# Optimization experiments

Hardware: AMD Instinct MI355X
Metric: run time of the kernel (lower is better)

The kernel has to match this reference:

```python
import jax, jax.numpy as jnp
import numpy as np

B, S, MM_DIM = 64, 512, 1024
HID, T, NL, NHEAD = 512, 4, 4, 8
DH = HID // NHEAD
RQ_L, CB = 3, 256
EPS = 1e-5


def setup_inputs() -> dict:
    key = jax.random.key(0)
    ks = jax.random.split(key, 24)
    n = jax.random.normal
    d = dict(
        multimodal_features=n(ks[0], (B, S, MM_DIM), jnp.float32),
        proj_W=n(ks[1], (MM_DIM, HID), jnp.float32) * 0.02,
        proj_b=jnp.zeros((HID,), jnp.float32),
        query_tokens=n(ks[2], (T, HID), jnp.float32),
        Wq=n(ks[3], (NL, HID, HID), jnp.float32) * 0.02,
        bq=jnp.zeros((NL, HID), jnp.float32),
        Wk=n(ks[4], (NL, HID, HID), jnp.float32) * 0.02,
        bk=jnp.zeros((NL, HID), jnp.float32),
        Wv=n(ks[5], (NL, HID, HID), jnp.float32) * 0.02,
        bv=jnp.zeros((NL, HID), jnp.float32),
        Wo=n(ks[6], (NL, HID, HID), jnp.float32) * 0.02,
        bo=jnp.zeros((NL, HID), jnp.float32),
        W1=n(ks[7], (NL, HID, 4 * HID), jnp.float32) * 0.02,
        b1=jnp.zeros((NL, 4 * HID), jnp.float32),
        W2=n(ks[8], (NL, 4 * HID, HID), jnp.float32) * 0.02,
        b2=jnp.zeros((NL, HID), jnp.float32),
        ln_g=jnp.ones((NL, HID), jnp.float32),
        ln_b=jnp.zeros((NL, HID), jnp.float32),
        codebooks=n(ks[9], (RQ_L, CB, HID), jnp.float32),
    )
    return d


def _layernorm(x, g, b):
    mu = jnp.mean(x, axis=-1, keepdims=True)
    var = jnp.mean(jnp.square(x - mu), axis=-1, keepdims=True)
    return (x - mu) * jax.lax.rsqrt(var + EPS) * g + b


def _cross_attn(q, kv, Wq, bq, Wk, bk, Wv, bv, Wo, bo):
    Bq, Tq, _ = q.shape
    Sk = kv.shape[1]
    qh = (q @ Wq + bq).reshape(Bq, Tq, NHEAD, DH)
    kh = (kv @ Wk + bk).reshape(Bq, Sk, NHEAD, DH)
    vh = (kv @ Wv + bv).reshape(Bq, Sk, NHEAD, DH)
    scores = jnp.einsum('bthd,bshd->bhts', qh, kh) / np.sqrt(DH).astype(np.float32)
    attn = jax.nn.softmax(scores, axis=-1)
    out = jnp.einsum('bhts,bshd->bthd', attn, vh).reshape(Bq, Tq, NHEAD * DH)
    return out @ Wo + bo


def reference(multimodal_features, proj_W, proj_b, query_tokens,
              Wq, bq, Wk, bk, Wv, bv, Wo, bo, W1, b1, W2, b2,
              ln_g, ln_b, codebooks):
    x = multimodal_features @ proj_W + proj_b            # [B,S,HID]
    q = jnp.broadcast_to(query_tokens[None], (x.shape[0], T, HID))
    for i in range(NL):
        attn = _cross_attn(q, x, Wq[i], bq[i], Wk[i], bk[i], Wv[i], bv[i], Wo[i], bo[i])
        q = _layernorm(q + attn, ln_g[i], ln_b[i])
        ffn = jax.nn.gelu(q @ W1[i] + b1[i], approximate=False) @ W2[i] + b2[i]
        q = _layernorm(q + ffn, ln_g[i], ln_b[i])
    # residual quantization
    residual = q
    reconstructed = jnp.zeros_like(q)
    ids = []
    for l in range(RQ_L):
        cb = codebooks[l]                                # [CB,HID]
        d2 = (jnp.sum(residual * residual, axis=-1, keepdims=True)
              - 2.0 * (residual @ cb.T)
              + jnp.sum(cb * cb, axis=-1))               # [B,T,CB]
        idx = jnp.argmin(d2, axis=-1)                    # [B,T]
        ids.append(idx)
        cent = cb[idx]                                   # gather [B,T,HID]
        reconstructed = reconstructed + cent
        residual = residual - cent
    semantic_ids = jnp.stack(ids, axis=-1)               # [B,T,RQ_L]
    return semantic_ids, reconstructed
```

## Files before the change

kernel.cpp:

```cpp
#include <hip/hip_runtime.h>
#include <math.h>


typedef __attribute__((ext_vector_type(8))) short   s16x8;
typedef __attribute__((ext_vector_type(8))) __bf16  bf16x8;
typedef __attribute__((ext_vector_type(4))) float   f32x4;

__device__ __forceinline__ void split2(float v, unsigned short& hi, unsigned short& lo) {
    unsigned u = __builtin_bit_cast(unsigned, v);
    hi = (unsigned short)(u >> 16);
    float hf = __builtin_bit_cast(float, u & 0xffff0000u);
    float l = v - hf;
    unsigned ul = __builtin_bit_cast(unsigned, l);
    lo = (unsigned short)((ul + 0x7fffu + ((ul >> 16) & 1u)) >> 16);
}

__device__ __forceinline__ f32x4 mfma16(bf16x8 a, bf16x8 b, f32x4 c) {
    return __builtin_amdgcn_mfma_f32_16x16x32_bf16(a, b, c, 0, 0, 0);
}

__device__ __forceinline__ void gload16(const void* g, void* l) {
    __builtin_amdgcn_global_load_lds(
        (const __attribute__((address_space(1))) unsigned*)g,
        (__attribute__((address_space(3))) unsigned*)l, 16, 0, 0);
}

__device__ __forceinline__ bf16x8 bc16(const unsigned short* p) {
    return __builtin_bit_cast(bf16x8, *(const s16x8*)p);
}

template<int BM, int FM, int FN, int WR, int WC, int AMODE, int OMODE,
         int IDX, bool GELU, bool SWZ>
__global__ __launch_bounds__(256)
void mfma_gemm(const void* __restrict__ Ah_, const void* __restrict__ Al_,
               const unsigned short* __restrict__ Bh_, const unsigned short* __restrict__ Bl_,
               const float* __restrict__ bias,
               void* __restrict__ Ch_, void* __restrict__ Cl_,
               int K, int lda, int ldb, int ldc,
               long strA, long strB, long strC)
{
    constexpr int BHALF = 8192;
    constexpr int AHALF = 2 * BM * 32;
    __shared__ __align__(16) unsigned short sA[2 * AHALF];
    __shared__ __align__(16) unsigned short sB[2 * BHALF];

    int bx = blockIdx.x, by = blockIdx.y;
    if constexpr (SWZ) {
        int nb = gridDim.x * gridDim.y;
        int h  = bx + gridDim.x * by;
        int orig = (h & 7) * (nb >> 3) + (h >> 3);
        bx = orig % gridDim.x; by = orig / gridDim.x;
    }
    const int tid = threadIdx.x, z = blockIdx.z;
    const int m0 = by * BM, n0 = bx * 128;
    const int lane = tid & 63, w = tid >> 6;
    const int wr = w / WC, wc = w % WC;

    const float* Af = nullptr;
    const unsigned short *Ah = nullptr, *Al = nullptr;
    if constexpr (AMODE == 1) {
        Af = (const float*)Ah_;
    } else {
        Ah = (const unsigned short*)Ah_ + (long)z * strA;
        Al = (const unsigned short*)Al_ + (long)z * strA;
    }
    const unsigned short* Bh = Bh_ + (long)z * strB;
    const unsigned short* Bl = Bl_ + (long)z * strB;

    auto stageB = [&](int buf, int k0) {
#pragma unroll
        for (int i = 0; i < 4; i++) {
            const int c = tid + 256 * i;
            const int p = c >> 9, cc = c & 511, r = cc >> 2, sl = cc & 3;
            const int fs = (r + (r >> 2)) & 3;
            const unsigned short* g = (p ? Bl : Bh) + (long)(n0 + r) * ldb + k0 + ((sl ^ fs)) * 8;
            gload16(g, sB + buf * BHALF + p * 4096 + r * 32 + sl * 8);
        }
    };
    auto stageA = [&](int buf, int k0) {
        if constexpr (AMODE == 0 && BM == 32) {
            const int p = tid >> 7, c = tid & 127, r = c >> 2, sl = c & 3;
            const int fs = (r + (r >> 2)) & 3;
            const unsigned short* g = (p ? Al : Ah) + (long)(m0 + r) * lda + k0 + ((sl ^ fs)) * 8;
            gload16(g, sA + buf * AHALF + p * (BM * 32) + r * 32 + sl * 8);
        } else if constexpr (AMODE == 0 && BM == 16) {
            if (tid < 128) {
                const int p = tid >> 6, c = tid & 63, r = c >> 2, sl = c & 3;
                const int fs = (r + (r >> 2)) & 3;
                const unsigned short* g = (p ? Al : Ah) + (long)(m0 + r) * lda + k0 + ((sl ^ fs)) * 8;
                gload16(g, sA + buf * AHALF + p * (BM * 32) + r * 32 + sl * 8);
            }
        } else {
            const int r = tid >> 1, hh2 = tid & 1;
            const int fs = (r + (r >> 2)) & 3;
            const float* src = Af + (long)(m0 + r) * lda + k0 + hh2 * 16;
#pragma unroll
            for (int s2 = 0; s2 < 2; s2++) {
                const int s = 2 * hh2 + s2;
                float4 v0 = *(const float4*)(src + s2 * 8);
                float4 v1 = *(const float4*)(src + s2 * 8 + 4);
                float vv[8] = {v0.x, v0.y, v0.z, v0.w, v1.x, v1.y, v1.z, v1.w};
                union { s16x8 v; unsigned short u[8]; } hu, lu;
#pragma unroll
                for (int j = 0; j < 8; j++) split2(vv[j], hu.u[j], lu.u[j]);
                *(s16x8*)&sA[buf * AHALF + r * 32 + ((s ^ fs)) * 8] = hu.v;
                *(s16x8*)&sA[buf * AHALF + BM * 32 + r * 32 + ((s ^ fs)) * 8] = lu.v;
            }
        }
    };

    f32x4 acc[FM][FN];
#pragma unroll
    for (int i = 0; i < FM; i++)
#pragma unroll
        for (int j = 0; j < FN; j++) acc[i][j] = f32x4{0.f, 0.f, 0.f, 0.f};

    const int NT = K / 32;
    int buf = 0;
    stageB(0, 0);
    stageA(0, 0);
    __syncthreads();

    const int li = lane & 15, ks = lane >> 4;

    for (int kt = 0; kt < NT; kt++) {
        if (kt + 1 < NT) { stageB(buf ^ 1, (kt + 1) * 32); stageA(buf ^ 1, (kt + 1) * 32); }
        bf16x8 ah[FM], al[FM], bh[FN], bl[FN];
#pragma unroll
        for (int mi = 0; mi < FM; mi++) {
            const int r = wr * (FM * 16) + mi * 16 + li;
            const int fs = (r + (r >> 2)) & 3;
            ah[mi] = bc16(&sA[buf * AHALF + r * 32 + ((ks ^ fs)) * 8]);
            al[mi] = bc16(&sA[buf * AHALF + BM * 32 + r * 32 + ((ks ^ fs)) * 8]);
        }
#pragma unroll
        for (int ni = 0; ni < FN; ni++) {
            const int r = wc * (FN * 16) + ni * 16 + li;
            const int fs = (r + (r >> 2)) & 3;
            bh[ni] = bc16(&sB[buf * BHALF + r * 32 + ((ks ^ fs)) * 8]);
            bl[ni] = bc16(&sB[buf * BHALF + 4096 + r * 32 + ((ks ^ fs)) * 8]);
        }
#pragma unroll
        for (int mi = 0; mi < FM; mi++)
#pragma unroll
            for (int ni = 0; ni < FN; ni++) acc[mi][ni] = mfma16(ah[mi], bh[ni], acc[mi][ni]);
#pragma unroll
        for (int mi = 0; mi < FM; mi++)
#pragma unroll
            for (int ni = 0; ni < FN; ni++) acc[mi][ni] = mfma16(ah[mi], bl[ni], acc[mi][ni]);
#pragma unroll
        for (int mi = 0; mi < FM; mi++)
#pragma unroll
            for (int ni = 0; ni < FN; ni++) acc[mi][ni] = mfma16(al[mi], bh[ni], acc[mi][ni]);
        __syncthreads();
        buf ^= 1;
    }

#pragma unroll
    for (int mi = 0; mi < FM; mi++)
#pragma unroll
        for (int r4 = 0; r4 < 4; r4++) {
            const int m = m0 + wr * (FM * 16) + mi * 16 + (lane >> 4) * 4 + r4;
#pragma unroll
            for (int ni = 0; ni < FN; ni++) {
                const int n = n0 + wc * (FN * 16) + ni * 16 + (lane & 15);
                float v = acc[mi][ni][r4];
                if (bias) v += bias[n];
                if constexpr (GELU) v = 0.5f * v * (1.f + erff(v * 0.70710678118654752f));
                long id;
                if constexpr (IDX == 0)      id = (long)z * strC + (long)m * ldc + n;
                else                         id = ((long)(m >> 2)) * 16384
                                                + (long)((n >> 9) * 4 + (m & 3)) * 512 + (n & 511);
                if constexpr (OMODE == 1) {
                    unsigned short h, l; split2(v, h, l);
                    ((unsigned short*)Ch_)[id] = h;
                    ((unsigned short*)Cl_)[id] = l;
                } else {
                    ((float*)Ch_)[id] = v;
                }
            }
        }
}

__global__ __launch_bounds__(512)
void fused_attn(const unsigned short* __restrict__ A_h, const unsigned short* __restrict__ A_l,
                const unsigned short* __restrict__ x_h, const unsigned short* __restrict__ x_l,
                const unsigned short* __restrict__ xT_h, const unsigned short* __restrict__ xT_l,
                unsigned short* __restrict__ U_h, unsigned short* __restrict__ U_l)
{
    __shared__ __align__(16) unsigned short sB[2][2][8192];
    __shared__ __align__(16) unsigned short sA[2][2][512];
    __shared__ __align__(16) unsigned short sP[2][16][16][32];
    __shared__ float redm[8][16], reds[8][16];

    const int tid = threadIdx.x;
    const int lin  = blockIdx.x + 2 * blockIdx.y;
    const int orig = (lin & 7) * 16 + (lin >> 3);
    const int b = orig >> 1, r0 = (orig & 1) * 16;
    const int lane = tid & 63, w = tid >> 6;
    const int li = lane & 15, ks = lane >> 4;
    const unsigned short* Ah = A_h + b * 16384 + r0 * 512;
    const unsigned short* Al = A_l + b * 16384 + r0 * 512;
    const unsigned short* xh = x_h + (long)b * 262144;
    const unsigned short* xl = x_l + (long)b * 262144;
    const unsigned short* xTh = xT_h + (long)b * 262144;
    const unsigned short* xTl = xT_l + (long)b * 262144;

    auto stage_B = [&](int buf, const unsigned short* sh, const unsigned short* sl2,
                       int row0, int k0) {
#pragma unroll
        for (int i = 0; i < 4; i++) {
            const int c2 = tid + 512 * i;
            const int p = c2 >> 10, cc = c2 & 1023, r = cc >> 2, sl = cc & 3;
            const int fs = (r + (r >> 2)) & 3;
            const unsigned short* g = (p ? sl2 : sh) + (long)(row0 + r) * 512 + k0 + (sl ^ fs) * 8;
            gload16(g, &sB[buf][p][r * 32 + sl * 8]);
        }
    };
    auto stage_A = [&](int buf, int k0) {
        if (tid < 128) {
            const int p = tid >> 6, c = tid & 63, r = c >> 2, sl = c & 3;
            const int fs = (r + (r >> 2)) & 3;
            const unsigned short* g = (p ? Al : Ah) + (long)r * 512 + k0 + (sl ^ fs) * 8;
            gload16(g, &sA[buf][p][r * 32 + sl * 8]);
        }
    };

    f32x4 acc[4];
#pragma unroll
    for (int i = 0; i < 4; i++) acc[i] = f32x4{0.f, 0.f, 0.f, 0.f};

    stage_B(0, xh, xl, 0, 0);
    stage_A(0, 0);
    __syncthreads();
    int buf = 0;
    const int fsa = (li + (li >> 2)) & 3;
    for (int t = 0; t < 32; t++) {
        const int half = t >> 4;
        const int nt = t + 1;
        if (nt < 32) {
            stage_B(buf ^ 1, xh, xl, (nt >> 4) * 256, (nt & 15) * 32);
            stage_A(buf ^ 1, (nt & 15) * 32);
        }
        bf16x8 ah = bc16(&sA[buf][0][li * 32 + ((ks ^ fsa)) * 8]);
        bf16x8 al = bc16(&sA[buf][1][li * 32 + ((ks ^ fsa)) * 8]);
        bf16x8 bh[2], bl[2];
#pragma unroll
        for (int ni = 0; ni < 2; ni++) {
            const int r = w * 32 + ni * 16 + li;
            const int fs = (r + (r >> 2)) & 3;
            bh[ni] = bc16(&sB[buf][0][r * 32 + ((ks ^ fs)) * 8]);
            bl[ni] = bc16(&sB[buf][1][r * 32 + ((ks ^ fs)) * 8]);
        }
#pragma unroll
        for (int ni = 0; ni < 2; ni++) acc[half * 2 + ni] = mfma16(ah, bh[ni], acc[half * 2 + ni]);
#pragma unroll
        for (int ni = 0; ni < 2; ni++) acc[half * 2 + ni] = mfma16(ah, bl[ni], acc[half * 2 + ni]);
#pragma unroll
        for (int ni = 0; ni < 2; ni++) acc[half * 2 + ni] = mfma16(al, bh[ni], acc[half * 2 + ni]);
        __syncthreads();
        buf ^= 1;
    }

    stage_B(buf, xTh, xTl, 0, 0);

    float M[4], S[4];
#pragma unroll
    for (int r4 = 0; r4 < 4; r4++) {
        float m = acc[0][r4];
#pragma unroll
        for (int i = 1; i < 4; i++) m = fmaxf(m, acc[i][r4]);
#pragma unroll
        for (int o = 1; o < 16; o <<= 1) m = fmaxf(m, __shfl_xor(m, o));
        M[r4] = m;
    }
    if (li == 0) {
#pragma unroll
        for (int r4 = 0; r4 < 4; r4++) redm[w][ks * 4 + r4] = M[r4];
    }
    __syncthreads();
#pragma unroll
    for (int r4 = 0; r4 < 4; r4++) {
        float m = redm[0][ks * 4 + r4];
#pragma unroll
        for (int ww = 1; ww < 8; ww++) m = fmaxf(m, redm[ww][ks * 4 + r4]);
        M[r4] = m;
    }
#pragma unroll
    for (int i = 0; i < 4; i++)
#pragma unroll
        for (int r4 = 0; r4 < 4; r4++) acc[i][r4] = expf(acc[i][r4] - M[r4]);
#pragma unroll
    for (int r4 = 0; r4 < 4; r4++) {
        float s = 0.f;
#pragma unroll
        for (int i = 0; i < 4; i++) s += acc[i][r4];
#pragma unroll
        for (int o = 1; o < 16; o <<= 1) s += __shfl_xor(s, o);
        S[r4] = s;
    }
    if (li == 0) {
#pragma unroll
        for (int r4 = 0; r4 < 4; r4++) reds[w][ks * 4 + r4] = S[r4];
    }
    __syncthreads();
#pragma unroll
    for (int r4 = 0; r4 < 4; r4++) {
        float s = 0.f;
#pragma unroll
        for (int ww = 0; ww < 8; ww++) s += reds[ww][ks * 4 + r4];
        S[r4] = 1.f / s;
    }
#pragma unroll
    for (int i = 0; i < 4; i++) {
        const int hf = i >> 1, ni = i & 1;
        const int s = hf * 256 + w * 32 + ni * 16 + li;
        const int kt = s >> 5, kks = (s >> 3) & 3, j = s & 7;
#pragma unroll
        for (int r4 = 0; r4 < 4; r4++) {
            const int row = ks * 4 + r4;
            const int fs = (row + (row >> 2)) & 3;
            unsigned short h, l2; split2(acc[i][r4] * S[r4], h, l2);
            sP[0][kt][row][(kks ^ fs) * 8 + j] = h;
            sP[1][kt][row][(kks ^ fs) * 8 + j] = l2;
        }
    }
    __syncthreads();

    f32x4 acc2[4];
#pragma unroll
    for (int i = 0; i < 4; i++) acc2[i] = f32x4{0.f, 0.f, 0.f, 0.f};
    for (int t = 0; t < 32; t++) {
        const int half = t >> 4, kt = t & 15;
        const int nt = t + 1;
        if (nt < 32) stage_B(buf ^ 1, xTh, xTl, (nt >> 4) * 256, (nt & 15) * 32);
        bf16x8 ph = bc16(&sP[0][kt][li][(ks ^ fsa) * 8]);
        bf16x8 pl = bc16(&sP[1][kt][li][(ks ^ fsa) * 8]);
        bf16x8 bh[2], bl[2];
#pragma unroll
        for (int ni = 0; ni < 2; ni++) {
            const int r = w * 32 + ni * 16 + li;
            const int fs = (r + (r >> 2)) & 3;
            bh[ni] = bc16(&sB[buf][0][r * 32 + ((ks ^ fs)) * 8]);
            bl[ni] = bc16(&sB[buf][1][r * 32 + ((ks ^ fs)) * 8]);
        }
#pragma unroll
        for (int ni = 0; ni < 2; ni++) acc2[half * 2 + ni] = mfma16(ph, bh[ni], acc2[half * 2 + ni]);
#pragma unroll
        for (int ni = 0; ni < 2; ni++) acc2[half * 2 + ni] = mfma16(ph, bl[ni], acc2[half * 2 + ni]);
#pragma unroll
        for (int ni = 0; ni < 2; ni++) acc2[half * 2 + ni] = mfma16(pl, bh[ni], acc2[half * 2 + ni]);
        __syncthreads();
        buf ^= 1;
    }

#pragma unroll
    for (int i = 0; i < 4; i++) {
        const int hf = i >> 1, ni = i & 1;
        const int n = hf * 256 + w * 32 + ni * 16 + li;
#pragma unroll
        for (int r4 = 0; r4 < 4; r4++) {
            const int m = r0 + ks * 4 + r4;
            const long id = ((long)b * 4 + (m & 3)) * 4096 + (long)(m >> 2) * 512 + n;
            unsigned short h, l2; split2(acc2[i][r4], h, l2);
            U_h[id] = h; U_l[id] = l2;
        }
    }
}

__global__ __launch_bounds__(256)
void ffn_fused(const unsigned short* __restrict__ q_h, const unsigned short* __restrict__ q_l,
               const unsigned short* __restrict__ W1T_h, const unsigned short* __restrict__ W1T_l,
               const float* __restrict__ b1,
               const unsigned short* __restrict__ W2T_h, const unsigned short* __restrict__ W2T_l,
               float* __restrict__ parts)
{
    __shared__ __align__(16) unsigned short sA[2 * 1024];
    __shared__ __align__(16) unsigned short sB[2 * 4096];
    __shared__ __align__(16) unsigned short sB2[8192];
    __shared__ __align__(16) unsigned short sF[2][2][16][32];
    const int cx = blockIdx.x, m0 = blockIdx.y * 16;
    const int tid = threadIdx.x, lane = tid & 63, w = tid >> 6;
    const int li = lane & 15, ks = lane >> 4;
    const int n0 = cx * 64;

    auto stageB1 = [&](int buf, int k0) {
#pragma unroll
        for (int i = 0; i < 2; i++) {
            const int c = tid + 256 * i;
            const int p = c >> 8, cc = c & 255, r = cc >> 2, sl = cc & 3;
            const int fs = (r + (r >> 2)) & 3;
            const unsigned short* g = (p ? W1T_l : W1T_h) + (long)(n0 + r) * 512 + k0 + (sl ^ fs) * 8;
            gload16(g, sB + buf * 4096 + p * 2048 + r * 32 + sl * 8);
        }
    };
    auto stageA1 = [&](int buf, int k0) {
        if (tid < 128) {
            const int p = tid >> 6, c = tid & 63, r = c >> 2, sl = c & 3;
            const int fs = (r + (r >> 2)) & 3;
            const unsigned short* g = (p ? q_l : q_h) + (long)(m0 + r) * 512 + k0 + (sl ^ fs) * 8;
            gload16(g, sA + buf * 1024 + p * 512 + r * 32 + sl * 8);
        }
    };

    f32x4 acc = f32x4{0.f, 0.f, 0.f, 0.f};
    int buf = 0;
    stageB1(0, 0); stageA1(0, 0);
    __syncthreads();
    const int fsa = (li + (li >> 2)) & 3;
    for (int kt = 0; kt < 16; kt++) {
        if (kt + 1 < 16) { stageB1(buf ^ 1, (kt + 1) * 32); stageA1(buf ^ 1, (kt + 1) * 32); }
        bf16x8 ah = bc16(sA + buf * 1024 + li * 32 + ((ks ^ fsa)) * 8);
        bf16x8 al = bc16(sA + buf * 1024 + 512 + li * 32 + ((ks ^ fsa)) * 8);
        const int r = w * 16 + li;
        const int fs = (r + (r >> 2)) & 3;
        bf16x8 bh = bc16(sB + buf * 4096 + r * 32 + ((ks ^ fs)) * 8);
        bf16x8 bl = bc16(sB + buf * 4096 + 2048 + r * 32 + ((ks ^ fs)) * 8);
        acc = mfma16(ah, bh, acc);
        acc = mfma16(ah, bl, acc);
        acc = mfma16(al, bh, acc);
        __syncthreads();
        buf ^= 1;
    }

#pragma unroll
    for (int r4 = 0; r4 < 4; r4++) {
        const int row = ks * 4 + r4;
        const int fs = (row + (row >> 2)) & 3;
        const int n = w * 16 + li;
        float v = acc[r4] + b1[n0 + n];
        v = 0.5f * v * (1.f + erff(v * 0.70710678118654752f));
        const int kt = n >> 5, kks = (n >> 3) & 3, j = n & 7;
        unsigned short h, l2; split2(v, h, l2);
        sF[0][kt][row][(kks ^ fs) * 8 + j] = h;
        sF[1][kt][row][(kks ^ fs) * 8 + j] = l2;
    }
    __syncthreads();

    for (int nc = 0; nc < 4; nc++) {
        f32x4 acc2[2];
#pragma unroll
        for (int j = 0; j < 2; j++) acc2[j] = f32x4{0.f, 0.f, 0.f, 0.f};
        for (int kt2 = 0; kt2 < 2; kt2++) {
            __syncthreads();
#pragma unroll
            for (int i = 0; i < 4; i++) {
                const int c = tid + 256 * i;
                const int p = c >> 9, cc = c & 511, r = cc >> 2, sl = cc & 3;
                const int fs = (r + (r >> 2)) & 3;
                const unsigned short* g = (p ? W2T_l : W2T_h)
                    + (long)(nc * 128 + r) * 2048 + cx * 64 + kt2 * 32 + (sl ^ fs) * 8;
                gload16(g, sB2 + p * 4096 + r * 32 + sl * 8);
            }
            __syncthreads();
            bf16x8 fh, fl, bh[2], bl[2];
            {
                const int row = li;
                const int fs = (row + (row >> 2)) & 3;
                fh = bc16(&sF[0][kt2][row][(ks ^ fs) * 8]);
                fl = bc16(&sF[1][kt2][row][(ks ^ fs) * 8]);
            }
#pragma unroll
            for (int ni = 0; ni < 2; ni++) {
                const int r = w * 32 + ni * 16 + li;
                const int fs = (r + (r >> 2)) & 3;
                bh[ni] = bc16(sB2 + r * 32 + (ks ^ fs) * 8);
                bl[ni] = bc16(sB2 + 4096 + r * 32 + (ks ^ fs) * 8);
            }
#pragma unroll
            for (int ni = 0; ni < 2; ni++) acc2[ni] = mfma16(fh, bh[ni], acc2[ni]);
#pragma unroll
            for (int ni = 0; ni < 2; ni++) acc2[ni] = mfma16(fh, bl[ni], acc2[ni]);
#pragma unroll
            for (int ni = 0; ni < 2; ni++) acc2[ni] = mfma16(fl, bh[ni], acc2[ni]);
        }
#pragma unroll
        for (int r4 = 0; r4 < 4; r4++) {
            const int m = m0 + ks * 4 + r4;
#pragma unroll
            for (int ni = 0; ni < 2; ni++) {
                const int n2 = nc * 128 + w * 32 + ni * 16 + li;
                parts[(long)cx * 131072 + (long)m * 512 + n2] = acc2[ni][r4];
            }
        }
    }
}


__device__ void prepT_body(float* t, int bx, int by, int z,
                           const float* __restrict__ in,
                           unsigned short* __restrict__ Th, unsigned short* __restrict__ Tl,
                           int ldin, int ldo, long inStride, long outStride)
{
    const int n0 = bx * 64, k0 = by * 64;
    const int tid = threadIdx.x;
    const float* src = in + (long)z * inStride;
#pragma unroll
    for (int i = 0; i < 4; i++) {
        int ch = tid + 256 * i;
        int r = ch >> 4, q = ch & 15;
        float4 v = *(const float4*)(src + (long)(k0 + r) * ldin + n0 + q * 4);
        t[r * 68 + q * 4 + 0] = v.x; t[r * 68 + q * 4 + 1] = v.y;
        t[r * 68 + q * 4 + 2] = v.z; t[r * 68 + q * 4 + 3] = v.w;
    }
    __syncthreads();
#pragma unroll
    for (int i = 0; i < 4; i++) {
        int ch = tid + 256 * i;
        int rc = ch >> 4, qk = ch & 15;
        union { uint2 v; unsigned short u[4]; } oh, ol;
#pragma unroll
        for (int j = 0; j < 4; j++) split2(t[(qk * 4 + j) * 68 + rc], oh.u[j], ol.u[j]);
        long o = (long)z * outStride + (long)(n0 + rc) * ldo + k0 + qk * 4;
        *(uint2*)(Th + o) = oh.v;
        *(uint2*)(Tl + o) = ol.v;
    }
}

__device__ void t32_body(float* t, int bx, int by, int z,
                         const float* __restrict__ in, float* __restrict__ out, long zstr)
{
    const int c0 = bx * 64, r0 = by * 64;
    const int tid = threadIdx.x;
#pragma unroll
    for (int i = 0; i < 4; i++) {
        int ch = tid + 256 * i;
        int r = ch >> 4, q = ch & 15;
        float4 v = *(const float4*)(in + (long)z * zstr + (long)(r0 + r) * 512 + c0 + q * 4);
        t[r * 65 + q * 4 + 0] = v.x; t[r * 65 + q * 4 + 1] = v.y;
        t[r * 65 + q * 4 + 2] = v.z; t[r * 65 + q * 4 + 3] = v.w;
    }
    __syncthreads();
#pragma unroll
    for (int i = 0; i < 4; i++) {
        int ch = tid + 256 * i;
        int rc = ch >> 4, qk = ch & 15;
        float4 o;
        o.x = t[(qk * 4 + 0) * 65 + rc]; o.y = t[(qk * 4 + 1) * 65 + rc];
        o.z = t[(qk * 4 + 2) * 65 + rc]; o.w = t[(qk * 4 + 3) * 65 + rc];
        *(float4*)(out + (long)z * zstr + (long)(c0 + rc) * 512 + r0 + qk * 4) = o;
    }
}

__global__ __launch_bounds__(256)
void big_prep(const float* projW, unsigned short* pwT_h, unsigned short* pwT_l,
              const float* W1, unsigned short* W1T_h, unsigned short* W1T_l,
              const float* W2, unsigned short* W2T_h, unsigned short* W2T_l,
              const float* Wo, float* WoT)
{
    __shared__ float t[64 * 68];
    const int bid = blockIdx.x;
    if (bid < 128) {
        prepT_body(t, bid & 7, bid >> 3, 0, projW, pwT_h, pwT_l, 512, 1024, 0, 0);
    } else if (bid < 1152) {
        int u = bid - 128;
        prepT_body(t, u & 31, (u >> 5) & 7, u >> 8, W1, W1T_h, W1T_l, 2048, 512, 1048576, 1048576);
    } else if (bid < 2176) {
        int u = bid - 1152;
        prepT_body(t, u & 7, (u >> 3) & 31, u >> 8, W2, W2T_h, W2T_l, 512, 2048, 1048576, 1048576);
    } else {
        int u = bid - 2176;
        t32_body(t, u & 7, (u >> 3) & 7, u >> 6, Wo, WoT, 262144);
    }
}

__device__ void w2_body(unsigned short* sA, unsigned short* sB, int bx, int by, int z,
                        const float* A_, const float* B_, float scale,
                        unsigned short* Th, unsigned short* Tl,
                        long zsA, long zsB, long S1, long S2, long SMs)
{
    const int tid = threadIdx.x;
    const int m0 = by * 128, n0 = bx * 128;
    const int lane = tid & 63, w = tid >> 6, wr = w >> 1, wc = w & 1;
    const float* Ab = A_ + (long)(z >> 3) * zsA + (z & 7) * 64;
    const float* Bb = B_ + (long)(z >> 3) * zsB + (z & 7) * 64;

    f32x4 acc[4][4];
#pragma unroll
    for (int i = 0; i < 4; i++)
#pragma unroll
        for (int j = 0; j < 4; j++) acc[i][j] = f32x4{0.f, 0.f, 0.f, 0.f};

    for (int k0 = 0; k0 < 64; k0 += 32) {
        __syncthreads();
#pragma unroll
        for (int op = 0; op < 2; op++) {
            const float* src0 = op ? Bb : Ab;
            unsigned short* dst = op ? sB : sA;
#pragma unroll
            for (int i = 0; i < 2; i++) {
                const int c = tid + 256 * i;
                const int r = c >> 2, s = c & 3;
                const int fs = (r + (r >> 2)) & 3;
                const float* src = src0 + (long)((op ? n0 : m0) + r) * 512 + k0 + s * 8;
                float4 v0 = *(const float4*)src;
                float4 v1 = *(const float4*)(src + 4);
                float vv[8] = {v0.x, v0.y, v0.z, v0.w, v1.x, v1.y, v1.z, v1.w};
                union { s16x8 v; unsigned short u[8]; } hh, ll;
#pragma unroll
                for (int j = 0; j < 8; j++) split2(vv[j], hh.u[j], ll.u[j]);
                *(s16x8*)&dst[0 * 4096 + r * 32 + (s ^ fs) * 8] = hh.v;
                *(s16x8*)&dst[1 * 4096 + r * 32 + (s ^ fs) * 8] = ll.v;
            }
        }
        __syncthreads();
        const int li = lane & 15, ks = lane >> 4;
        bf16x8 ah[4], al[4], bh[4], bl[4];
#pragma unroll
        for (int mi = 0; mi < 4; mi++) {
            const int r = wr * 64 + mi * 16 + li;
            const int fs = (r + (r >> 2)) & 3;
            ah[mi] = bc16(sA + r * 32 + (ks ^ fs) * 8);
            al[mi] = bc16(sA + 4096 + r * 32 + (ks ^ fs) * 8);
        }
#pragma unroll
        for (int ni = 0; ni < 4; ni++) {
            const int r = wc * 64 + ni * 16 + li;
            const int fs = (r + (r >> 2)) & 3;
            bh[ni] = bc16(sB + r * 32 + (ks ^ fs) * 8);
            bl[ni] = bc16(sB + 4096 + r * 32 + (ks ^ fs) * 8);
        }
#pragma unroll
        for (int mi = 0; mi < 4; mi++)
#pragma unroll
            for (int ni = 0; ni < 4; ni++) acc[mi][ni] = mfma16(ah[mi], bh[ni], acc[mi][ni]);
#pragma unroll
        for (int mi = 0; mi < 4; mi++)
#pragma unroll
            for (int ni = 0; ni < 4; ni++) acc[mi][ni] = mfma16(ah[mi], bl[ni], acc[mi][ni]);
#pragma unroll
        for (int mi = 0; mi < 4; mi++)
#pragma unroll
            for (int ni = 0; ni < 4; ni++) acc[mi][ni] = mfma16(al[mi], bh[ni], acc[mi][ni]);
    }
#pragma unroll
    for (int mi = 0; mi < 4; mi++)
#pragma unroll
        for (int r4 = 0; r4 < 4; r4++) {
            const int m = m0 + wr * 64 + mi * 16 + (lane >> 4) * 4 + r4;
#pragma unroll
            for (int ni = 0; ni < 4; ni++) {
                const int n = n0 + wc * 64 + ni * 16 + (lane & 15);
                float v = acc[mi][ni][r4] * scale;
                unsigned short h, l; split2(v, h, l);
                long id = (long)(z >> 3) * S1 + (long)(z & 7) * S2 + (long)m * SMs + n;
                Th[id] = h; Tl[id] = l;
            }
        }
}

__global__ __launch_bounds__(256)
void w2_merged(const float* Wk, const float* Wq,
               unsigned short* MT_h, unsigned short* MT_l,
               const float* WoT, const float* Wv,
               unsigned short* WVOT_h, unsigned short* WVOT_l)
{
    __shared__ __align__(16) unsigned short sA[2 * 4096];
    __shared__ __align__(16) unsigned short sB[2 * 4096];
    const int bid = blockIdx.x;
    if (bid < 512) {
        w2_body(sA, sB, bid & 3, (bid >> 2) & 3, bid >> 4, Wk, Wq, 0.125f, MT_h, MT_l,
                262144, 262144, 2097152, 262144, 512);
    } else {
        int u = bid - 512;
        w2_body(sA, sB, u & 3, (u >> 2) & 3, u >> 4, WoT, Wv, 1.f, WVOT_h, WVOT_l,
                262144, 262144, 2097152, 512, 4096);
    }
}

__global__ __launch_bounds__(256)
void small_prep(const float* cbook, float* cbT, float* cn,
                const float* bq, const float* Wk, float* biasA,
                const float* bv, const float* Wo, const float* bo, float* biasO,
                const float* qt, float* q, unsigned short* qh_s, unsigned short* ql_s)
{
    __shared__ float sm[256];
    const int bid = blockIdx.x, tid = threadIdx.x;
    if (bid < 768) {
        const int rowi = bid, l = rowi >> 8, j = rowi & 255;
        const float* row = cbook + (long)rowi * 512;
        float v0 = row[tid], v1 = row[tid + 256];
        cbT[(long)l * 131072 + (long)tid * 256 + j]         = v0;
        cbT[(long)l * 131072 + (long)(tid + 256) * 256 + j] = v1;
        float s = v0 * v0 + v1 * v1;
#pragma unroll
        for (int o = 32; o > 0; o >>= 1) s += __shfl_xor(s, o);
        if ((tid & 63) == 0) sm[tid >> 6] = s;
        __syncthreads();
        if (tid == 0) cn[rowi] = sm[0] + sm[1] + sm[2] + sm[3];
    } else if (bid < 832) {
        const int gid = (bid - 768) * 256 + tid;
        const int l = gid >> 12, hc = gid & 4095, h = hc >> 9, c = hc & 511;
        const float* b = bq + l * 512 + h * 64;
        const float* w = Wk + (long)l * 262144 + (long)c * 512 + h * 64;
        float s = 0.f;
#pragma unroll 16
        for (int d = 0; d < 64; d++) s = fmaf(b[d], w[d], s);
        biasA[gid] = 0.125f * s;
    } else if (bid < 864) {
        const int u = bid - 832;
        const int l = u >> 3, oc = u & 7;
        const int o = oc * 64 + (tid & 63), j4 = tid >> 6;
        float acc = 0.f;
        for (int j = j4; j < 512; j += 4)
            acc = fmaf(bv[l * 512 + j], Wo[(long)l * 262144 + (long)j * 512 + o], acc);
        sm[j4 * 64 + (tid & 63)] = acc;
        __syncthreads();
        if (tid < 64) {
            float s = sm[tid] + sm[64 + tid] + sm[128 + tid] + sm[192 + tid]
                    + bo[l * 512 + oc * 64 + tid];
            biasO[l * 512 + oc * 64 + tid] = s;
        }
    } else {
        const int r = bid - 864, t = r & 3;
        const long base = (long)r * 512;
        float a = qt[t * 512 + tid], c = qt[t * 512 + 256 + tid];
        q[base + tid] = a; q[base + 256 + tid] = c;
        unsigned short h, l;
        split2(a, h, l); qh_s[base + tid] = h;       ql_s[base + tid] = l;
        split2(c, h, l); qh_s[base + tid + 256] = h; ql_s[base + tid + 256] = l;
    }
}

__global__ __launch_bounds__(256) void transpose_x(const unsigned short* __restrict__ xh,
                                                   const unsigned short* __restrict__ xl,
                                                   unsigned short* __restrict__ xTh,
                                                   unsigned short* __restrict__ xTl)
{
    __shared__ unsigned short th[64][72], tl[64][72];
    const int b = blockIdx.z, c0 = blockIdx.x * 64, s0 = blockIdx.y * 64;
    const int tid = threadIdx.x;
    const long ibase = ((long)b * 512 + s0) * 512 + c0;
#pragma unroll
    for (int i = 0; i < 2; i++) {
        int ch = tid + 256 * i;
        int r = ch >> 3, s = ch & 7;
        *(s16x8*)&th[r][s * 8] = *(const s16x8*)(xh + ibase + (long)r * 512 + s * 8);
        *(s16x8*)&tl[r][s * 8] = *(const s16x8*)(xl + ibase + (long)r * 512 + s * 8);
    }
    __syncthreads();
    const long obase = ((long)b * 512 + c0) * 512 + s0;
#pragma unroll
    for (int i = 0; i < 2; i++) {
        int ch = tid + 256 * i;
        int rc = ch >> 3, sc = ch & 7;
        union { s16x8 v; unsigned short u[8]; } oh, ol;
#pragma unroll
        for (int j = 0; j < 8; j++) { oh.u[j] = th[sc * 8 + j][rc]; ol.u[j] = tl[sc * 8 + j][rc]; }
        *(s16x8*)(xTh + obase + (long)rc * 512 + sc * 8) = oh.v;
        *(s16x8*)(xTl + obase + (long)rc * 512 + sc * 8) = ol.v;
    }
}

__global__ __launch_bounds__(256) void add_ln_sum(float* __restrict__ q,
                                                  const float* __restrict__ parts, int np,
                                                  const float* __restrict__ bias,
                                                  const float* __restrict__ g,
                                                  const float* __restrict__ b,
                                                  unsigned short* __restrict__ qh_s,
                                                  unsigned short* __restrict__ ql_s)
{
    __shared__ float red[4];
    const int tid = threadIdx.x;
    const long base = (long)blockIdx.x * 512;
    float* row = q + base;
    float v0 = row[tid] + bias[tid];
    float v1 = row[tid + 256] + bias[tid + 256];
    for (int z = 0; z < np; z++) {
        v0 += parts[(long)z * 131072 + base + tid];
        v1 += parts[(long)z * 131072 + base + tid + 256];
    }
    float s = v0 + v1;
#pragma unroll
    for (int o = 32; o > 0; o >>= 1) s += __shfl_xor(s, o);
    if ((tid & 63) == 0) red[tid >> 6] = s;
    __syncthreads();
    float mu = (red[0] + red[1] + red[2] + red[3]) * (1.f / 512.f);
    __syncthreads();
    float c0 = v0 - mu, c1 = v1 - mu;
    float sq = c0 * c0 + c1 * c1;
#pragma unroll
    for (int o = 32; o > 0; o >>= 1) sq += __shfl_xor(sq, o);
    if ((tid & 63) == 0) red[tid >> 6] = sq;
    __syncthreads();
    float var = (red[0] + red[1] + red[2] + red[3]) * (1.f / 512.f);
    float rs = rsqrtf(var + 1e-5f);
    float o0 = c0 * rs * g[tid] + b[tid];
    float o1 = c1 * rs * g[tid + 256] + b[tid + 256];
    row[tid] = o0; row[tid + 256] = o1;
    unsigned short h, l;
    split2(o0, h, l); qh_s[base + tid] = h;       ql_s[base + tid] = l;
    split2(o1, h, l); qh_s[base + tid + 256] = h; ql_s[base + tid + 256] = l;
}

__global__ __launch_bounds__(256) void rq_kernel(const float* __restrict__ qf,
                                                 const float* __restrict__ cb,
                                                 const float* __restrict__ cbT,
                                                 const float* __restrict__ cn,
                                                 float* __restrict__ out)
{
    __shared__ float r[512], rec[512];
    __shared__ float rd[4]; __shared__ int ri[4];
    __shared__ int sids[3];
    const int p = blockIdx.x, tid = threadIdx.x;
    r[tid]         = qf[(long)p * 512 + tid];
    r[tid + 256]   = qf[(long)p * 512 + 256 + tid];
    rec[tid] = 0.f; rec[tid + 256] = 0.f;
    __syncthreads();
    for (int l = 0; l < 3; l++) {
        const float* ct = cbT + (long)l * 131072;
        float dot = 0.f;
#pragma unroll 8
        for (int k = 0; k < 512; k++) dot = fmaf(r[k], ct[(long)k * 256 + tid], dot);
        float d2 = cn[l * 256 + tid] - 2.f * dot;
        int idx = tid;
#pragma unroll
        for (int o = 32; o > 0; o >>= 1) {
            float od = __shfl_xor(d2, o); int oi = __shfl_xor(idx, o);
            if (od < d2 || (od == d2 && oi < idx)) { d2 = od; idx = oi; }
        }
        if ((tid & 63) == 0) { rd[tid >> 6] = d2; ri[tid >> 6] = idx; }
        __syncthreads();
        if (tid == 0) {
            float bd = rd[0]; int bb = ri[0];
            for (int w = 1; w < 4; w++)
                if (rd[w] < bd || (rd[w] == bd && ri[w] < bb)) { bd = rd[w]; bb = ri[w]; }
            sids[l] = bb;
        }
        __syncthreads();
        const float* crow = cb + ((long)l * 256 + sids[l]) * 512;
        float c0 = crow[tid], c1 = crow[tid + 256];
        r[tid] -= c0; rec[tid] += c0;
        r[tid + 256] -= c1; rec[tid + 256] += c1;
        __syncthreads();
    }
    float* orec = out + 768 + (long)p * 512;
    orec[tid] = rec[tid]; orec[tid + 256] = rec[tid + 256];
    if (tid < 3) out[p * 3 + tid] = (float)sids[tid];
}

extern "C" void kernel_launch(void* const* d_in, const int* in_sizes, int n_in,
                              void* d_out, int out_size, void* d_ws, size_t ws_size,
                              hipStream_t stream)
{
    const float* mm    = (const float*)d_in[0];
    const float* projW = (const float*)d_in[1];
    const float* projb = (const float*)d_in[2];
    const float* qt    = (const float*)d_in[3];
    const float* Wq    = (const float*)d_in[4];
    const float* bq    = (const float*)d_in[5];
    const float* Wk    = (const float*)d_in[6];
    const float* Wv    = (const float*)d_in[8];
    const float* bv    = (const float*)d_in[9];
    const float* Wo    = (const float*)d_in[10];
    const float* bo    = (const float*)d_in[11];
    const float* W1    = (const float*)d_in[12];
    const float* b1    = (const float*)d_in[13];
    const float* W2    = (const float*)d_in[14];
    const float* b2    = (const float*)d_in[15];
    const float* lng   = (const float*)d_in[16];
    const float* lnb   = (const float*)d_in[17];
    const float* cbook = (const float*)d_in[18];

    char* p = (char*)d_ws;
    auto alloc = [&](size_t bytes) { char* r = p; p += (bytes + 255) & ~(size_t)255; return r; };
    unsigned short* x_h   = (unsigned short*)alloc(16777216ull * 2);
    unsigned short* x_l   = (unsigned short*)alloc(16777216ull * 2);
    unsigned short* xT_h  = (unsigned short*)alloc(16777216ull * 2);
    unsigned short* xT_l  = (unsigned short*)alloc(16777216ull * 2);
    unsigned short* pwT_h = (unsigned short*)alloc(524288ull * 2);
    unsigned short* pwT_l = (unsigned short*)alloc(524288ull * 2);
    unsigned short* MT_h  = (unsigned short*)alloc(8388608ull * 2);
    unsigned short* MT_l  = (unsigned short*)alloc(8388608ull * 2);
    unsigned short* WVOT_h= (unsigned short*)alloc(8388608ull * 2);
    unsigned short* WVOT_l= (unsigned short*)alloc(8388608ull * 2);
    float*          WoT   = (float*)alloc(1048576ull * 4);
    unsigned short* W1T_h = (unsigned short*)alloc(4194304ull * 2);
    unsigned short* W1T_l = (unsigned short*)alloc(4194304ull * 2);
    unsigned short* W2T_h = (unsigned short*)alloc(4194304ull * 2);
    unsigned short* W2T_l = (unsigned short*)alloc(4194304ull * 2);
    unsigned short* A_h   = (unsigned short*)alloc(1048576ull * 2);
    unsigned short* A_l   = (unsigned short*)alloc(1048576ull * 2);
    unsigned short* U_h   = (unsigned short*)alloc(1048576ull * 2);
    unsigned short* U_l   = (unsigned short*)alloc(1048576ull * 2);
    unsigned short* q_h   = (unsigned short*)alloc(131072ull * 2);
    unsigned short* q_l   = (unsigned short*)alloc(131072ull * 2);
    float* parts = (float*)alloc(32ull * 131072 * 4);
    float* q     = (float*)alloc(131072ull * 4);
    float* cbT   = (float*)alloc(393216ull * 4);
    float* cn    = (float*)alloc(768ull * 4);
    float* biasA = (float*)alloc(16384ull * 4);
    float* biasO = (float*)alloc(2048ull * 4);

    big_prep<<<2432, 256, 0, stream>>>(projW, pwT_h, pwT_l, W1, W1T_h, W1T_l,
                                       W2, W2T_h, W2T_l, Wo, WoT);
    w2_merged<<<1024, 256, 0, stream>>>(Wk, Wq, MT_h, MT_l, WoT, Wv, WVOT_h, WVOT_l);
    small_prep<<<1120, 256, 0, stream>>>(cbook, cbT, cn, bq, Wk, biasA,
                                         bv, Wo, bo, biasO, qt, q, q_h, q_l);

    mfma_gemm<128, 4, 4, 2, 2, 1, 1, 0, false, true><<<dim3(4, 256, 1), 256, 0, stream>>>(
        mm, nullptr, pwT_h, pwT_l, projb, x_h, x_l, 1024, 1024, 1024, 512, 0, 0, 0);
    transpose_x<<<dim3(8, 8, 64), 256, 0, stream>>>(x_h, x_l, xT_h, xT_l);

    for (int i = 0; i < 4; i++) {
        const unsigned short* MTh = MT_h + (long)i * 2097152;
        const unsigned short* MTl = MT_l + (long)i * 2097152;
        const unsigned short* WVh = WVOT_h + (long)i * 2097152;
        const unsigned short* WVl = WVOT_l + (long)i * 2097152;
        const unsigned short* W1h = W1T_h + (long)i * 1048576;
        const unsigned short* W1l = W1T_l + (long)i * 1048576;
        const unsigned short* W2h = W2T_h + (long)i * 1048576;
        const unsigned short* W2l = W2T_l + (long)i * 1048576;
        const float* b1i = b1 + i * 2048; const float* b2i = b2 + i * 512;
        const float* gi  = lng + i * 512; const float* bi_ = lnb + i * 512;

        mfma_gemm<16, 1, 2, 1, 4, 0, 1, 1, false, false><<<dim3(32, 16, 1), 256, 0, stream>>>(
            q_h, q_l, MTh, MTl, biasA + i * 4096, A_h, A_l, 512, 512, 512, 512, 0, 0, 0);
        fused_attn<<<dim3(2, 64), 512, 0, stream>>>(A_h, A_l, x_h, x_l, xT_h, xT_l, U_h, U_l);
        mfma_gemm<16, 1, 2, 1, 4, 0, 0, 0, false, false><<<dim3(4, 16, 8), 256, 0, stream>>>(
            U_h, U_l, WVh, WVl, nullptr, parts, nullptr, 512, 4096, 4096, 512,
            512, 512, 131072);
        add_ln_sum<<<256, 256, 0, stream>>>(q, parts, 8, biasO + i * 512, gi, bi_, q_h, q_l);
        ffn_fused<<<dim3(32, 16), 256, 0, stream>>>(q_h, q_l, W1h, W1l, b1i, W2h, W2l, parts);
        add_ln_sum<<<256, 256, 0, stream>>>(q, parts, 32, b2i, gi, bi_, q_h, q_l);
    }

    rq_kernel<<<256, 256, 0, stream>>>(q, cbook, cbT, cn, (float*)d_out);
}
```

Baseline: 864.9 us.

## Pre-split input to bf16 pairs and fuse transposed x write into projection GEMM

The fp32 multimodal features are now split into hi/lo bf16 planes by a separate prep kernel, so the projection GEMM can stage A through direct global-to-LDS loads instead of converting fp32 in registers each tile. The projection GEMM epilogue also writes the transposed x planes directly, which removes the separate transpose kernel. Weight prep buffers are aliased into the same scratch region as the split input, with the weight prep moved after the projection. The split adds a full extra read and write pass over the 128 MB input, and the transposed epilogue stores are 8-byte scattered writes.

Result: slower. 906.3 us (+4.8%).

```diff
diff --git a/kernel.cpp b/kernel.cpp
--- a/kernel.cpp
+++ b/kernel.cpp
@@ -30,14 +30,15 @@
 }
 
 template<int BM, int FM, int FN, int WR, int WC, int AMODE, int OMODE,
-         int IDX, bool GELU, bool SWZ>
+         int IDX, bool GELU, bool SWZ, bool XTW>
 __global__ __launch_bounds__(256)
 void mfma_gemm(const void* __restrict__ Ah_, const void* __restrict__ Al_,
                const unsigned short* __restrict__ Bh_, const unsigned short* __restrict__ Bl_,
                const float* __restrict__ bias,
                void* __restrict__ Ch_, void* __restrict__ Cl_,
                int K, int lda, int ldb, int ldc,
-               long strA, long strB, long strC)
+               long strA, long strB, long strC,
+               unsigned short* __restrict__ xTh_, unsigned short* __restrict__ xTl_)
 {
     constexpr int BHALF = 8192;
     constexpr int AHALF = 2 * BM * 32;
@@ -56,14 +57,8 @@
     const int lane = tid & 63, w = tid >> 6;
     const int wr = w / WC, wc = w % WC;
 
-    const float* Af = nullptr;
-    const unsigned short *Ah = nullptr, *Al = nullptr;
-    if constexpr (AMODE == 1) {
-        Af = (const float*)Ah_;
-    } else {
-        Ah = (const unsigned short*)Ah_ + (long)z * strA;
-        Al = (const unsigned short*)Al_ + (long)z * strA;
-    }
+    const unsigned short* Ah = (const unsigned short*)Ah_ + (long)z * strA;
+    const unsigned short* Al = (const unsigned short*)Al_ + (long)z * strA;
     const unsigned short* Bh = Bh_ + (long)z * strB;
     const unsigned short* Bl = Bl_ + (long)z * strB;
 
@@ -78,34 +73,27 @@
         }
     };
     auto stageA = [&](int buf, int k0) {
-        if constexpr (AMODE == 0 && BM == 32) {
+        if constexpr (BM == 128) {
+#pragma unroll
+            for (int i = 0; i < 4; i++) {
+                const int c = tid + 256 * i;
+                const int p = c >> 9, cc = c & 511, r = cc >> 2, sl = cc & 3;
+                const int fs = (r + (r >> 2)) & 3;
+                const unsigned short* g = (p ? Al : Ah) + (long)(m0 + r) * lda + k0 + ((sl ^ fs)) * 8;
+                gload16(g, sA + buf * AHALF + p * (BM * 32) + r * 32 + sl * 8);
+            }
+        } else if constexpr (BM == 32) {
             const int p = tid >> 7, c = tid & 127, r = c >> 2, sl = c & 3;
             const int fs = (r + (r >> 2)) & 3;
             const unsigned short* g = (p ? Al : Ah) + (long)(m0 + r) * lda + k0 + ((sl ^ fs)) * 8;
             gload16(g, sA + buf * AHALF + p * (BM * 32) + r * 32 + sl * 8);
-        } else if constexpr (AMODE == 0 && BM == 16) {
+        } else {
             if (tid < 128) {
                 const int p = tid >> 6, c = tid & 63, r = c >> 2, sl = c & 3;
                 const int fs = (r + (r >> 2)) & 3;
                 const unsigned short* g = (p ? Al : Ah) + (long)(m0 + r) * lda + k0 + ((sl ^ fs)) * 8;
                 gload16(g, sA + buf * AHALF + p * (BM * 32) + r * 32 + sl * 8);
             }
-        } else {
-            const int r = tid >> 1, hh2 = tid & 1;
-            const int fs = (r + (r >> 2)) & 3;
-            const float* src = Af + (long)(m0 + r) * lda + k0 + hh2 * 16;
-#pragma unroll
-            for (int s2 = 0; s2 < 2; s2++) {
-                const int s = 2 * hh2 + s2;
-                float4 v0 = *(const float4*)(src + s2 * 8);
-                float4 v1 = *(const float4*)(src + s2 * 8 + 4);
-                float vv[8] = {v0.x, v0.y, v0.z, v0.w, v1.x, v1.y, v1.z, v1.w};
-                union { s16x8 v; unsigned short u[8]; } hu, lu;
-#pragma unroll
-                for (int j = 0; j < 8; j++) split2(vv[j], hu.u[j], lu.u[j]);
-                *(s16x8*)&sA[buf * AHALF + r * 32 + ((s ^ fs)) * 8] = hu.v;
-                *(s16x8*)&sA[buf * AHALF + BM * 32 + r * 32 + ((s ^ fs)) * 8] = lu.v;
-            }
         }
     };
 
@@ -159,11 +147,13 @@
 #pragma unroll
     for (int mi = 0; mi < FM; mi++)
 #pragma unroll
-        for (int r4 = 0; r4 < 4; r4++) {
-            const int m = m0 + wr * (FM * 16) + mi * 16 + (lane >> 4) * 4 + r4;
-#pragma unroll
-            for (int ni = 0; ni < FN; ni++) {
-                const int n = n0 + wc * (FN * 16) + ni * 16 + (lane & 15);
+        for (int ni = 0; ni < FN; ni++) {
+            const int n = n0 + wc * (FN * 16) + ni * 16 + (lane & 15);
+            const int mb = m0 + wr * (FM * 16) + mi * 16 + (lane >> 4) * 4;
+            unsigned short hx[4], lx[4];
+#pragma unroll
+            for (int r4 = 0; r4 < 4; r4++) {
+                const int m = mb + r4;
                 float v = acc[mi][ni][r4];
                 if (bias) v += bias[n];
                 if constexpr (GELU) v = 0.5f * v * (1.f + erff(v * 0.70710678118654752f));
@@ -175,9 +165,19 @@
                     unsigned short h, l; split2(v, h, l);
                     ((unsigned short*)Ch_)[id] = h;
                     ((unsigned short*)Cl_)[id] = l;
+                    hx[r4] = h; lx[r4] = l;
                 } else {
                     ((float*)Ch_)[id] = v;
                 }
+            }
+            if constexpr (XTW) {
+                const int b = mb >> 9, s = mb & 511;
+                const long o = (long)b * 262144 + (long)n * 512 + s;
+                union { uint2 v; unsigned short u[4]; } ph, pl;
+#pragma unroll
+                for (int j = 0; j < 4; j++) { ph.u[j] = hx[j]; pl.u[j] = lx[j]; }
+                *(uint2*)(xTh_ + o) = ph.v;
+                *(uint2*)(xTl_ + o) = pl.v;
             }
         }
 }
@@ -543,23 +543,47 @@
 }
 
 __global__ __launch_bounds__(256)
-void big_prep(const float* projW, unsigned short* pwT_h, unsigned short* pwT_l,
-              const float* W1, unsigned short* W1T_h, unsigned short* W1T_l,
-              const float* W2, unsigned short* W2T_h, unsigned short* W2T_l,
-              const float* Wo, float* WoT)
+void pre_prep(const float* __restrict__ mm, unsigned short* __restrict__ mm_h,
+              unsigned short* __restrict__ mm_l,
+              const float* __restrict__ projW, unsigned short* __restrict__ pwT_h,
+              unsigned short* __restrict__ pwT_l)
 {
     __shared__ float t[64 * 68];
     const int bid = blockIdx.x;
-    if (bid < 128) {
-        prepT_body(t, bid & 7, bid >> 3, 0, projW, pwT_h, pwT_l, 512, 1024, 0, 0);
-    } else if (bid < 1152) {
-        int u = bid - 128;
-        prepT_body(t, u & 31, (u >> 5) & 7, u >> 8, W1, W1T_h, W1T_l, 2048, 512, 1048576, 1048576);
-    } else if (bid < 2176) {
-        int u = bid - 1152;
+    if (bid < 4096) {
+        const long gt = (long)bid * 256 + threadIdx.x;
+#pragma unroll
+        for (int j = 0; j < 4; j++) {
+            const long off = (gt + (long)j * 1048576) * 8;
+            float4 v0 = *(const float4*)(mm + off);
+            float4 v1 = *(const float4*)(mm + off + 4);
+            float vv[8] = {v0.x, v0.y, v0.z, v0.w, v1.x, v1.y, v1.z, v1.w};
+            union { s16x8 v; unsigned short u[8]; } hh, ll;
+#pragma unroll
+            for (int k = 0; k < 8; k++) split2(vv[k], hh.u[k], ll.u[k]);
+            *(s16x8*)(mm_h + off) = hh.v;
+            *(s16x8*)(mm_l + off) = ll.v;
+        }
+    } else {
+        int u = bid - 4096;
+        prepT_body(t, u & 7, u >> 3, 0, projW, pwT_h, pwT_l, 512, 1024, 0, 0);
+    }
+}
+
+__global__ __launch_bounds__(256)
+void post_prep(const float* W1, unsigned short* W1T_h, unsigned short* W1T_l,
+               const float* W2, unsigned short* W2T_h, unsigned short* W2T_l,
+               const float* Wo, float* WoT)
+{
+    __shared__ float t[64 * 68];
+    const int bid = blockIdx.x;
+    if (bid < 1024) {
+        prepT_body(t, bid & 31, (bid >> 5) & 7, bid >> 8, W1, W1T_h, W1T_l, 2048, 512, 1048576, 1048576);
+    } else if (bid < 2048) {
+        int u = bid - 1024;
         prepT_body(t, u & 7, (u >> 3) & 31, u >> 8, W2, W2T_h, W2T_l, 512, 2048, 1048576, 1048576);
     } else {
-        int u = bid - 2176;
+        int u = bid - 2048;
         t32_body(t, u & 7, (u >> 3) & 7, u >> 6, Wo, WoT, 262144);
     }
 }
@@ -722,36 +746,6 @@
     }
 }
 
-__global__ __launch_bounds__(256) void transpose_x(const unsigned short* __restrict__ xh,
-                                                   const unsigned short* __restrict__ xl,
-                                                   unsigned short* __restrict__ xTh,
-                                                   unsigned short* __restrict__ xTl)
-{
-    __shared__ unsigned short th[64][72], tl[64][72];
-    const int b = blockIdx.z, c0 = blockIdx.x * 64, s0 = blockIdx.y * 64;
-    const int tid = threadIdx.x;
-    const long ibase = ((long)b * 512 + s0) * 512 + c0;
-#pragma unroll
-    for (int i = 0; i < 2; i++) {
-        int ch = tid + 256 * i;
-        int r = ch >> 3, s = ch & 7;
-        *(s16x8*)&th[r][s * 8] = *(const s16x8*)(xh + ibase + (long)r * 512 + s * 8);
-        *(s16x8*)&tl[r][s * 8] = *(const s16x8*)(xl + ibase + (long)r * 512 + s * 8);
-    }
-    __syncthreads();
-    const long obase = ((long)b * 512 + c0) * 512 + s0;
-#pragma unroll
-    for (int i = 0; i < 2; i++) {
-        int ch = tid + 256 * i;
-        int rc = ch >> 3, sc = ch & 7;
-        union { s16x8 v; unsigned short u[8]; } oh, ol;
-#pragma unroll
-        for (int j = 0; j < 8; j++) { oh.u[j] = th[sc * 8 + j][rc]; ol.u[j] = tl[sc * 8 + j][rc]; }
-        *(s16x8*)(xTh + obase + (long)rc * 512 + sc * 8) = oh.v;
-        *(s16x8*)(xTl + obase + (long)rc * 512 + sc * 8) = ol.v;
-    }
-}
-
 __global__ __launch_bounds__(256) void add_ln_sum(float* __restrict__ q,
                                                   const float* __restrict__ parts, int np,
                                                   const float* __restrict__ bias,
@@ -864,21 +858,26 @@
 
     char* p = (char*)d_ws;
     auto alloc = [&](size_t bytes) { char* r = p; p += (bytes + 255) & ~(size_t)255; return r; };
+
+    char* X = alloc(134217728ull);
+    unsigned short* mm_h  = (unsigned short*)X;
+    unsigned short* mm_l  = (unsigned short*)(X + 67108864);
+    float*          WoT   = (float*)X;
+    unsigned short* W1T_h = (unsigned short*)(X + 4194304);
+    unsigned short* W1T_l = (unsigned short*)(X + 12582912);
+    unsigned short* W2T_h = (unsigned short*)(X + 20971520);
+    unsigned short* W2T_l = (unsigned short*)(X + 29360128);
+    unsigned short* MT_h  = (unsigned short*)(X + 37748736);
+    unsigned short* MT_l  = (unsigned short*)(X + 54525952);
+    unsigned short* WVOT_h= (unsigned short*)(X + 71303168);
+    unsigned short* WVOT_l= (unsigned short*)(X + 88080384);
+
     unsigned short* x_h   = (unsigned short*)alloc(16777216ull * 2);
     unsigned short* x_l   = (unsigned short*)alloc(16777216ull * 2);
     unsigned short* xT_h  = (unsigned short*)alloc(16777216ull * 2);
     unsigned short* xT_l  = (unsigned short*)alloc(16777216ull * 2);
     unsigned short* pwT_h = (unsigned short*)alloc(524288ull * 2);
     unsigned short* pwT_l = (unsigned short*)alloc(524288ull * 2);
-    unsigned short* MT_h  = (unsigned short*)alloc(8388608ull * 2);
-    unsigned short* MT_l  = (unsigned short*)alloc(8388608ull * 2);
-    unsigned short* WVOT_h= (unsigned short*)alloc(8388608ull * 2);
-    unsigned short* WVOT_l= (unsigned short*)alloc(8388608ull * 2);
-    float*          WoT   = (float*)alloc(1048576ull * 4);
-    unsigned short* W1T_h = (unsigned short*)alloc(4194304ull * 2);
-    unsigned short* W1T_l = (unsigned short*)alloc(4194304ull * 2);
-    unsigned short* W2T_h = (unsigned short*)alloc(4194304ull * 2);
-    unsigned short* W2T_l = (unsigned short*)alloc(4194304ull * 2);
     unsigned short* A_h   = (unsigned short*)alloc(1048576ull * 2);
     unsigned short* A_l   = (unsigned short*)alloc(1048576ull * 2);
     unsigned short* U_h   = (unsigned short*)alloc(1048576ull * 2);
@@ -892,15 +891,13 @@
     float* biasA = (float*)alloc(16384ull * 4);
     float* biasO = (float*)alloc(2048ull * 4);
 
-    big_prep<<<2432, 256, 0, stream>>>(projW, pwT_h, pwT_l, W1, W1T_h, W1T_l,
-                                       W2, W2T_h, W2T_l, Wo, WoT);
+    pre_prep<<<4224, 256, 0, stream>>>(mm, mm_h, mm_l, projW, pwT_h, pwT_l);
+    mfma_gemm<128, 4, 4, 2, 2, 0, 1, 0, false, true, true><<<dim3(4, 256, 1), 256, 0, stream>>>(
+        mm_h, mm_l, pwT_h, pwT_l, projb, x_h, x_l, 1024, 1024, 1024, 512, 0, 0, 0, xT_h, xT_l);
+    post_prep<<<2304, 256, 0, stream>>>(W1, W1T_h, W1T_l, W2, W2T_h, W2T_l, Wo, WoT);
     w2_merged<<<1024, 256, 0, stream>>>(Wk, Wq, MT_h, MT_l, WoT, Wv, WVOT_h, WVOT_l);
     small_prep<<<1120, 256, 0, stream>>>(cbook, cbT, cn, bq, Wk, biasA,
                                          bv, Wo, bo, biasO, qt, q, q_h, q_l);
-
-    mfma_gemm<128, 4, 4, 2, 2, 1, 1, 0, false, true><<<dim3(4, 256, 1), 256, 0, stream>>>(
-        mm, nullptr, pwT_h, pwT_l, projb, x_h, x_l, 1024, 1024, 1024, 512, 0, 0, 0);
-    transpose_x<<<dim3(8, 8, 64), 256, 0, stream>>>(x_h, x_l, xT_h, xT_l);
 
     for (int i = 0; i < 4; i++) {
         const unsigned short* MTh = MT_h + (long)i * 2097152;
@@ -914,12 +911,13 @@
         const float* b1i = b1 + i * 2048; const float* b2i = b2 + i * 512;
         const float* gi  = lng + i * 512; const float* bi_ = lnb + i * 512;
 
-        mfma_gemm<16, 1, 2, 1, 4, 0, 1, 1, false, false><<<dim3(32, 16, 1), 256, 0, stream>>>(
-            q_h, q_l, MTh, MTl, biasA + i * 4096, A_h, A_l, 512, 512, 512, 512, 0, 0, 0);
+        mfma_gemm<16, 1, 2, 1, 4, 0, 1, 1, false, false, false><<<dim3(32, 16, 1), 256, 0, stream>>>(
+            q_h, q_l, MTh, MTl, biasA + i * 4096, A_h, A_l, 512, 512, 512, 512, 0, 0, 0,
+            nullptr, nullptr);
         fused_attn<<<dim3(2, 64), 512, 0, stream>>>(A_h, A_l, x_h, x_l, xT_h, xT_l, U_h, U_l);
-        mfma_gemm<16, 1, 2, 1, 4, 0, 0, 0, false, false><<<dim3(4, 16, 8), 256, 0, stream>>>(
+        mfma_gemm<16, 1, 2, 1, 4, 0, 0, 0, false, false, false><<<dim3(4, 16, 8), 256, 0, stream>>>(
             U_h, U_l, WVh, WVl, nullptr, parts, nullptr, 512, 4096, 4096, 512,
-            512, 512, 131072);
+            512, 512, 131072, nullptr, nullptr);
         add_ln_sum<<<256, 256, 0, stream>>>(q, parts, 8, biasO + i * 512, gi, bi_, q_h, q_l);
         ffn_fused<<<dim3(32, 16), 256, 0, stream>>>(q_h, q_l, W1h, W1l, b1i, W2h, W2l, parts);
         add_ln_sum<<<256, 256, 0, stream>>>(q, parts, 32, b2i, gi, bi_, q_h, q_l);
```
